# Kernel optimization log

Hardware: AMD Instinct MI355X
Metric: run time of the kernel (lower is better)

Reference implementation:

```python
import jax, jax.numpy as jnp
from jax import lax
import numpy as np

B, P, E, DX = 32, 1024, 32, 5
FLAT = 24576  # 16*3*512 from the conv stack on 224x224 input


def _glorot(key, shape):
    fan_in = shape[-2] if len(shape) == 2 else shape[0] * shape[1] * shape[2]
    fan_out = shape[-1]
    std = jnp.sqrt(2.0 / (fan_in + fan_out))
    return jax.random.normal(key, shape, dtype=jnp.float32) * std


def setup_inputs() -> dict:
    key = jax.random.key(0)
    ks = jax.random.split(key, 20)
    d = {
        'image': jax.random.normal(ks[0], (B, 224, 224, 3), dtype=jnp.float32),
        'particles': jax.random.normal(ks[1], (B, P, DX), dtype=jnp.float32),
        'w1': _glorot(ks[2], (7, 7, 3, 128)),   'b1': jnp.zeros((128,), jnp.float32),
        'w2': _glorot(ks[3], (5, 5, 128, 128)), 'b2': jnp.zeros((128,), jnp.float32),
        'w3': _glorot(ks[4], (3, 3, 128, 256)), 'b3': jnp.zeros((256,), jnp.float32),
        'w4': _glorot(ks[5], (3, 3, 256, 256)), 'b4': jnp.zeros((256,), jnp.float32),
        'w5': _glorot(ks[6], (3, 3, 256, 512)), 'b5': jnp.zeros((512,), jnp.float32),
        'fc1_w': _glorot(ks[7], (FLAT, 1024)),  'fc1_b': jnp.zeros((1024,), jnp.float32),
        'fc2_w': _glorot(ks[8], (1024, 512)),   'fc2_b': jnp.zeros((512,), jnp.float32),
        'fc4_w': _glorot(ks[9], (512, 128)),    'fc4_b': jnp.zeros((128,), jnp.float32),
        'lk1_w': _glorot(ks[10], (128, 128)),   'lk1_b': jnp.zeros((128,), jnp.float32),
        'lk2_w': _glorot(ks[11], (128, 32)),    'lk2_b': jnp.zeros((32,), jnp.float32),
        'lk3_w': _glorot(ks[12], (32, 1)),      'lk3_b': jnp.zeros((1,), jnp.float32),
        'pr1_w': _glorot(ks[13], (2, 32)),      'pr1_b': jnp.zeros((32,), jnp.float32),
        'pr2_w': _glorot(ks[14], (32, 64)),     'pr2_b': jnp.zeros((64,), jnp.float32),
        'pr3_w': _glorot(ks[15], (64, 2)),      'pr3_b': jnp.zeros((2,), jnp.float32),
    }
    return d


def _conv_relu(x, w, b, strides):
    y = lax.conv_general_dilated(x, w, strides, 'VALID',
                                 dimension_numbers=('NHWC', 'HWIO', 'NHWC'))
    return jax.nn.relu(y + b)


def _bn(x):
    # fresh BatchNormalization created in call(): gamma=1, beta=0, batch stats, eps=1e-3
    m = jnp.mean(x, axis=(0, 1, 2))
    v = jnp.var(x, axis=(0, 1, 2))
    return (x - m) * lax.rsqrt(v + 1e-3)


def _forward(image, particles, w1, b1, w2, b2, w3, b3, w4, b4, w5, b5,
             fc1_w, fc1_b, fc2_w, fc2_b, fc4_w, fc4_b,
             lk1_w, lk1_b, lk2_w, lk2_b, lk3_w, lk3_b,
             pr1_w, pr1_b, pr2_w, pr2_b, pr3_w, pr3_b):
    # ---- sensor model (CNN) ----
    c = _bn(_conv_relu(image, w1, b1, (3, 3)))
    c = _bn(_conv_relu(c, w2, b2, (1, 2)))
    c = _bn(_conv_relu(c, w3, b3, (1, 2)))
    c = _bn(_conv_relu(c, w4, b4, (2, 2)))
    c = _bn(_conv_relu(c, w5, b5, (2, 2)))          # [B,16,3,512]
    flat = c.reshape(B, -1)                          # [B, FLAT]
    # per-batch tile to ensemble members (vectorized replacement of the Python loop)
    z = jnp.repeat(flat, E, axis=0)                  # [B*E, FLAT]
    h = jax.nn.relu(z @ fc1_w + fc1_b)
    h = jax.nn.relu(h @ fc2_w + fc2_b)
    h = jax.nn.relu(h @ fc4_w + fc4_b)               # DenseFlipout ~ deterministic mean kernel
    encoding = h.reshape(B, E, 128).mean(axis=1)     # [B,128]
    # ---- likelihood ----
    encp = jnp.repeat(encoding, P, axis=0)           # [B*P,128]
    l = jax.nn.relu(encp @ lk1_w + lk1_b)
    l = jax.nn.relu(l @ lk2_w + lk2_b)
    l = jax.nn.sigmoid(l @ lk3_w + lk3_b)            # [B*P,1]
    like = l.reshape(B, P)
    like = like / jnp.sum(like, axis=1, keepdims=True)
    # ---- process model ----
    s = particles.reshape(B * P, DX)
    theta = s[:, 2:3] + s[:, 4:5]
    v = s[:, 3:4]
    theta_dot = s[:, 4:5]
    x = s[:, 0:1] + v * jnp.sin(theta)
    y = s[:, 1:2] + v * jnp.cos(theta)
    din = jnp.concatenate([v, theta_dot], axis=-1)   # [B*P,2]
    u = jax.nn.relu(din @ pr1_w + pr1_b)
    u = jax.nn.relu(u @ pr2_w + pr2_b)
    u = jnp.tanh(u @ pr3_w + pr3_b)
    dout = din + u
    new_state = jnp.concatenate([x, y, theta, dout], axis=-1).reshape(B, P, DX)
    return new_state, like


def reference(image, particles, w1, b1, w2, b2, w3, b3, w4, b4, w5, b5,
              fc1_w, fc1_b, fc2_w, fc2_b, fc4_w, fc4_b,
              lk1_w, lk1_b, lk2_w, lk2_b, lk3_w, lk3_b,
              pr1_w, pr1_b, pr2_w, pr2_b, pr3_w, pr3_b):
    return _forward(image, particles, w1, b1, w2, b2, w3, b3, w4, b4, w5, b5,
                    fc1_w, fc1_b, fc2_w, fc2_b, fc4_w, fc4_b,
                    lk1_w, lk1_b, lk2_w, lk2_b, lk3_w, lk3_b,
                    pr1_w, pr1_b, pr2_w, pr2_b, pr3_w, pr3_b)
```

## Files before the change

### kernel.cpp

```cpp
#include <hip/hip_runtime.h>
#include <math.h>

#define B   32
#define P   1024
#define DX  5
#define BP  (B * P)
#define LIKE_OFF (BP * DX)


#define PPW 8
#define NWAVES (BP / PPW)
#define BLOCKS (NWAVES / 4)

__device__ __forceinline__ float fast_tanh(float x) {
    x = fminf(fmaxf(x, -15.0f), 15.0f);
    float e = __expf(2.0f * x);
    return (e - 1.0f) / (e + 1.0f);
}

__global__ __launch_bounds__(256, 4) void particle_kernel(
    const float* __restrict__ particles,
    const float* __restrict__ pr1_w,
    const float* __restrict__ pr1_b,
    const float* __restrict__ pr2_w,
    const float* __restrict__ pr2_b,
    const float* __restrict__ pr3_w,
    const float* __restrict__ pr3_b,
    float* __restrict__ out)
{
    const int lane = threadIdx.x & 63;
    const int ws   = threadIdx.x >> 6;
    const int wid  = blockIdx.x * 4 + ws;

    float w2col[32];
#pragma unroll
    for (int k = 0; k < 32; ++k) w2col[k] = pr2_w[k * 64 + lane];
    const float  b2j = pr2_b[lane];
    const float2 w3  = reinterpret_cast<const float2*>(pr3_w)[lane];
    float w1a = 0.0f, w1b = 0.0f, w1c = 0.0f;
    if (lane < 32) {
        w1a = pr1_w[lane];
        w1b = pr1_w[32 + lane];
        w1c = pr1_b[lane];
    }
    const float b3a = pr3_b[0];
    const float b3b = pr3_b[1];

    __shared__ __align__(16) float h1s[4][32];

    for (int p = 0; p < PPW; ++p) {
        const int idx = wid * PPW + p;

        const float* s = particles + idx * DX;
        const float s0 = s[0];
        const float s1 = s[1];
        const float s2 = s[2];
        const float v  = s[3];
        const float td = s[4];

        const float theta = s2 + td;
        const float x = fmaf(v, __sinf(theta), s0);
        const float y = fmaf(v, __cosf(theta), s1);

        const float h1 = fmaxf(fmaf(v, w1a, fmaf(td, w1b, w1c)), 0.0f);
        if (lane < 32) h1s[ws][lane] = h1;

        float acc = b2j;
        const float4* h4 = reinterpret_cast<const float4*>(h1s[ws]);
#pragma unroll
        for (int k4 = 0; k4 < 8; ++k4) {
            const float4 h = h4[k4];
            acc = fmaf(h.x, w2col[k4 * 4 + 0], acc);
            acc = fmaf(h.y, w2col[k4 * 4 + 1], acc);
            acc = fmaf(h.z, w2col[k4 * 4 + 2], acc);
            acc = fmaf(h.w, w2col[k4 * 4 + 3], acc);
        }
        const float h2 = fmaxf(acc, 0.0f);

        float u0 = h2 * w3.x;
        float u1 = h2 * w3.y;
#pragma unroll
        for (int m = 1; m < 64; m <<= 1) {
            u0 += __shfl_xor(u0, m, 64);
            u1 += __shfl_xor(u1, m, 64);
        }
        u0 = fast_tanh(u0 + b3a);
        u1 = fast_tanh(u1 + b3b);

        if (lane < 6) {
            const float val = (lane == 0) ? x
                            : (lane == 1) ? y
                            : (lane == 2) ? theta
                            : (lane == 3) ? (v + u0)
                            : (lane == 4) ? (td + u1)
                            : (1.0f / 1024.0f);
            float* addr = (lane < 5) ? (out + idx * DX + lane)
                                     : (out + LIKE_OFF + idx);
            *addr = val;
        }
    }
}

extern "C" void kernel_launch(void* const* d_in, const int* in_sizes, int n_in,
                              void* d_out, int out_size, void* d_ws, size_t ws_size,
                              hipStream_t stream) {
    const float* particles = (const float*)d_in[1];
    const float* pr1_w = (const float*)d_in[24];
    const float* pr1_b = (const float*)d_in[25];
    const float* pr2_w = (const float*)d_in[26];
    const float* pr2_b = (const float*)d_in[27];
    const float* pr3_w = (const float*)d_in[28];
    const float* pr3_b = (const float*)d_in[29];
    float* out = (float*)d_out;

    dim3 grid(BLOCKS);
    dim3 block(256);
    particle_kernel<<<grid, block, 0, stream>>>(
        particles, pr1_w, pr1_b, pr2_w, pr2_b, pr3_w, pr3_b, out);
}
```

Baseline: 15.16 us.

## Preload particle states, split layer-1 and layer-2 phases, halve shuffle reductions

Each wave now loads all 8 of its particle states up front through a wave-uniform base address. It computes layer-1 activations for all 8 particles into shared memory in a first pass, then runs layer 2, 3 and the output stores in a second pass. The two-output reduction is merged into one shuffle chain: an initial xor-1 exchange places each output on alternating lanes, which roughly halves the shuffle count. The aim is to remove the per-particle load latency and the shared-memory dependency stalls, at the cost of more registers and shared memory.

```diff
diff --git a/kernel.cpp b/kernel.cpp
--- a/kernel.cpp
+++ b/kernel.cpp
@@ -43,30 +43,41 @@
         w1b = pr1_w[32 + lane];
         w1c = pr1_b[lane];
     }
-    const float b3a = pr3_b[0];
-    const float b3b = pr3_b[1];
+    const float b3 = (lane & 1) ? pr3_b[1] : pr3_b[0];
 
-    __shared__ __align__(16) float h1s[4][32];
+    const int pbase = __builtin_amdgcn_readfirstlane(wid * (PPW * DX));
+    float ps[PPW * DX];
+#pragma unroll
+    for (int i = 0; i < PPW * DX; ++i) ps[i] = particles[pbase + i];
 
+    __shared__ float h1s[4][PPW][32];
+
+#pragma unroll
     for (int p = 0; p < PPW; ++p) {
-        const int idx = wid * PPW + p;
+        const float s0 = ps[p * 5 + 0];
+        const float s1 = ps[p * 5 + 1];
+        const float s2 = ps[p * 5 + 2];
+        const float v  = ps[p * 5 + 3];
+        const float td = ps[p * 5 + 4];
+        const float theta = s2 + td;
 
-        const float* s = particles + idx * DX;
-        const float s0 = s[0];
-        const float s1 = s[1];
-        const float s2 = s[2];
-        const float v  = s[3];
-        const float td = s[4];
+        if (lane < 32)
+            h1s[ws][p][lane] = fmaxf(fmaf(v, w1a, fmaf(td, w1b, w1c)), 0.0f);
 
-        const float theta = s2 + td;
-        const float x = fmaf(v, __sinf(theta), s0);
-        const float y = fmaf(v, __cosf(theta), s1);
+        if (lane < 3) {
+            const float val = (lane == 0) ? fmaf(v, __sinf(theta), s0)
+                            : (lane == 1) ? fmaf(v, __cosf(theta), s1)
+                            : theta;
+            out[(wid * PPW + p) * DX + lane] = val;
+        }
+    }
 
-        const float h1 = fmaxf(fmaf(v, w1a, fmaf(td, w1b, w1c)), 0.0f);
-        if (lane < 32) h1s[ws][lane] = h1;
+    if (lane < PPW) out[LIKE_OFF + wid * PPW + lane] = 1.0f / 1024.0f;
 
+#pragma unroll
+    for (int p = 0; p < PPW; ++p) {
+        const float4* h4 = reinterpret_cast<const float4*>(h1s[ws][p]);
         float acc = b2j;
-        const float4* h4 = reinterpret_cast<const float4*>(h1s[ws]);
 #pragma unroll
         for (int k4 = 0; k4 < 8; ++k4) {
             const float4 h = h4[k4];
@@ -77,26 +88,20 @@
         }
         const float h2 = fmaxf(acc, 0.0f);
 
-        float u0 = h2 * w3.x;
-        float u1 = h2 * w3.y;
+        const float a0 = h2 * w3.x;
+        const float a1 = h2 * w3.y;
+        const bool odd = (lane & 1);
+        float mine   = odd ? a1 : a0;
+        float theirs = odd ? a0 : a1;
+        mine += __shfl_xor(theirs, 1, 64);
 #pragma unroll
-        for (int m = 1; m < 64; m <<= 1) {
-            u0 += __shfl_xor(u0, m, 64);
-            u1 += __shfl_xor(u1, m, 64);
-        }
-        u0 = fast_tanh(u0 + b3a);
-        u1 = fast_tanh(u1 + b3b);
+        for (int m = 2; m < 64; m <<= 1) mine += __shfl_xor(mine, m, 64);
 
-        if (lane < 6) {
-            const float val = (lane == 0) ? x
-                            : (lane == 1) ? y
-                            : (lane == 2) ? theta
-                            : (lane == 3) ? (v + u0)
-                            : (lane == 4) ? (td + u1)
-                            : (1.0f / 1024.0f);
-            float* addr = (lane < 5) ? (out + idx * DX + lane)
-                                     : (out + LIKE_OFF + idx);
-            *addr = val;
+        const float t = fast_tanh(mine + b3);
+
+        if (lane < 2) {
+            const float val = ((lane == 0) ? ps[p * 5 + 3] : ps[p * 5 + 4]) + t;
+            out[(wid * PPW + p) * DX + 3 + lane] = val;
         }
     }
 }
```

New measurement: 13.15 us. 1.15x faster.
